# Kernel optimization log

Hardware: AMD Instinct MI355X
Metric: run time of the kernel (lower is better)

Reference implementation:

```python
import jax, jax.numpy as jnp
import numpy as np

B, C, W, H, D = 2, 256, 32, 32, 32
CH = C // 2  # 128
LN_EPS = 1e-5


def _spatial_pool(x, wm, bm):
    # x: [B,C,W,H,D]; wm: [C]; bm: scalar. 1x1x1 conv C->1 == channel dot.
    b, c = x.shape[0], x.shape[1]
    xf = x.reshape(b, c, -1)                       # [B,C,N]
    mask = jnp.einsum('bcn,c->bn', xf, wm) + bm    # [B,N]
    attn = jax.nn.softmax(mask, axis=1)            # softmax over spatial N
    return jnp.einsum('bcn,bn->bc', xf, attn)      # [B,C] weighted-sum pool


def _channel_add(ctx, w1, b1, g, be, w2, b2):
    # 1x1 conv C->C/2, LayerNorm over C/2, ReLU, 1x1 conv C/2->C
    h = ctx @ w1.T + b1                            # [B,CH]
    mu = jnp.mean(h, axis=-1, keepdims=True)
    var = jnp.mean((h - mu) ** 2, axis=-1, keepdims=True)
    h = (h - mu) * jax.lax.rsqrt(var + LN_EPS) * g + be
    h = jax.nn.relu(h)
    return h @ w2.T + b2                           # [B,C]


def setup_inputs() -> dict:
    key = jax.random.key(0)
    ks = jax.random.split(key, 20)
    s = 0.02
    d = {
        'preds_S': jax.random.normal(ks[0], (B, C, W, H, D), jnp.float32),
        'preds_T': jax.random.normal(ks[1], (B, C, W, H, D), jnp.float32),
        'wm_s': jax.random.normal(ks[2], (C,), jnp.float32) * s,
        'bm_s': jnp.zeros((), jnp.float32),
        'wm_t': jax.random.normal(ks[3], (C,), jnp.float32) * s,
        'bm_t': jnp.zeros((), jnp.float32),
        'w1_s': jax.random.normal(ks[4], (CH, C), jnp.float32) * s,
        'b1_s': jnp.zeros((CH,), jnp.float32),
        'g_s': jnp.ones((CH,), jnp.float32),
        'be_s': jnp.zeros((CH,), jnp.float32),
        'w2_s': jax.random.normal(ks[5], (C, CH), jnp.float32) * s,
        'b2_s': jnp.zeros((C,), jnp.float32),
        'w1_t': jax.random.normal(ks[6], (CH, C), jnp.float32) * s,
        'b1_t': jnp.zeros((CH,), jnp.float32),
        'g_t': jnp.ones((CH,), jnp.float32),
        'be_t': jnp.zeros((CH,), jnp.float32),
        'w2_t': jax.random.normal(ks[7], (C, CH), jnp.float32) * s,
        'b2_t': jnp.zeros((C,), jnp.float32),
    }
    return d


def reference(preds_S, preds_T, wm_s, bm_s, wm_t, bm_t,
              w1_s, b1_s, g_s, be_s, w2_s, b2_s,
              w1_t, b1_t, g_t, be_t, w2_t, b2_t):
    ctx_s = _spatial_pool(preds_S, wm_s, bm_s)     # [B,C]
    ctx_t = _spatial_pool(preds_T, wm_t, bm_t)
    add_s = _channel_add(ctx_s, w1_s, b1_s, g_s, be_s, w2_s, b2_s)  # [B,C]
    add_t = _channel_add(ctx_t, w1_t, b1_t, g_t, be_t, w2_t, b2_t)
    out_s = preds_S + add_s[:, :, None, None, None]
    out_t = preds_T + add_t[:, :, None, None, None]
    diff = out_s - out_t
    return jnp.sum(diff * diff) / preds_S.shape[0]
```

## Files before the change

kernel.cpp:

```cpp
#include <hip/hip_runtime.h>
#include <math.h>
#include <limits.h>

#define Bc   2
#define Cc   256
#define Nn   32768
#define CHc  128
#define NPC  8
#define CPB  (Cc / NPC)
#define NT   1024
#define NTILES (Nn / NT)
#define LN_EPS 1e-5f

__device__ __forceinline__ int enc_f(float f) {
  int i = __float_as_int(f);
  return i >= 0 ? i : (i ^ 0x7FFFFFFF);
}
__device__ __forceinline__ float dec_f(int k) {
  return __int_as_float(k >= 0 ? k : (k ^ 0x7FFFFFFF));
}

__global__ __launch_bounds__(256) void gc_k1_mask(
    const float* __restrict__ S, const float* __restrict__ T,
    const float* __restrict__ wms, const float* __restrict__ wmt,
    float* __restrict__ mp, int* __restrict__ Mkey,
    float* __restrict__ sumsq) {
  const int tile = blockIdx.x;
  const int b    = blockIdx.y;
  const int pc   = blockIdx.z;
  const int tid  = threadIdx.x;

  if (tile == 0 && b == 0 && pc == 0) {
    if (tid < 4) Mkey[tid] = INT_MIN;
    if (tid == 4) *sumsq = 0.f;
  }

  const int n0 = tile * NT + tid * 4;
  const int c0 = pc * CPB;

  const float* Sp = S + ((size_t)b * Cc + c0) * Nn + n0;
  const float* Tp = T + ((size_t)b * Cc + c0) * Nn + n0;

  float4 as = make_float4(0.f, 0.f, 0.f, 0.f);
  float4 at = make_float4(0.f, 0.f, 0.f, 0.f);

#pragma unroll 8
  for (int i = 0; i < CPB; ++i) {
    const float ws = wms[c0 + i];
    const float wt = wmt[c0 + i];
    const float4 s = *(const float4*)(Sp + (size_t)i * Nn);
    const float4 t = *(const float4*)(Tp + (size_t)i * Nn);
    as.x += ws * s.x; as.y += ws * s.y; as.z += ws * s.z; as.w += ws * s.w;
    at.x += wt * t.x; at.y += wt * t.y; at.z += wt * t.z; at.w += wt * t.w;
  }

  float* outS = mp + (((size_t)0 * NPC + pc) * Bc + b) * Nn + n0;
  float* outT = mp + (((size_t)1 * NPC + pc) * Bc + b) * Nn + n0;
  *(float4*)outS = as;
  *(float4*)outT = at;
}

__global__ __launch_bounds__(256) void gc_k2a_combine(
    const float* __restrict__ mp, const float* __restrict__ bms,
    const float* __restrict__ bmt, float* __restrict__ mask,
    int* __restrict__ Mkey) {
  const int tile = blockIdx.x;
  const int b    = blockIdx.y;
  const int tt   = blockIdx.z;
  const int tid  = threadIdx.x;
  const int n0   = tile * NT + tid * 4;

  const float bm = (tt ? bmt : bms)[0];
  float4 m = make_float4(bm, bm, bm, bm);
#pragma unroll
  for (int pc = 0; pc < NPC; ++pc) {
    const float4 p =
        *(const float4*)(mp + (((size_t)tt * NPC + pc) * Bc + b) * Nn + n0);
    m.x += p.x; m.y += p.y; m.z += p.z; m.w += p.w;
  }
  *(float4*)(mask + ((size_t)tt * Bc + b) * Nn + n0) = m;

  float lmax = fmaxf(fmaxf(m.x, m.y), fmaxf(m.z, m.w));
  __shared__ float red[256];
  red[tid] = lmax;
  __syncthreads();
  for (int s = 128; s > 0; s >>= 1) {
    if (tid < s) red[tid] = fmaxf(red[tid], red[tid + s]);
    __syncthreads();
  }
  if (tid == 0) atomicMax(&Mkey[tt * Bc + b], enc_f(red[0]));
}

__global__ __launch_bounds__(256) void gc_k3_pool(
    const float* __restrict__ S, const float* __restrict__ T,
    const float* __restrict__ mask, const int* __restrict__ Mkey,
    float* __restrict__ ctx, float* __restrict__ rowsum,
    float* __restrict__ sumsq) {
  const int c   = blockIdx.x;
  const int b   = blockIdx.y;
  const int tid = threadIdx.x;

  const float M1 = dec_f(Mkey[0 * Bc + b]);
  const float M2 = dec_f(Mkey[1 * Bc + b]);

  const float* Sp = S + ((size_t)b * Cc + c) * Nn;
  const float* Tp = T + ((size_t)b * Cc + c) * Nn;
  const float* m1 = mask + ((size_t)0 * Bc + b) * Nn;
  const float* m2 = mask + ((size_t)1 * Bc + b) * Nn;

  float cs = 0.f, ct = 0.f, te1 = 0.f, te2 = 0.f, rs = 0.f, sq = 0.f;
  for (int n = tid * 4; n < Nn; n += 1024) {
    const float4 s = *(const float4*)(Sp + n);
    const float4 t = *(const float4*)(Tp + n);
    const float4 a = *(const float4*)(m1 + n);
    const float4 g = *(const float4*)(m2 + n);
    const float e1x = __expf(a.x - M1), e1y = __expf(a.y - M1),
                e1z = __expf(a.z - M1), e1w = __expf(a.w - M1);
    const float e2x = __expf(g.x - M2), e2y = __expf(g.y - M2),
                e2z = __expf(g.z - M2), e2w = __expf(g.w - M2);
    cs += s.x * e1x + s.y * e1y + s.z * e1z + s.w * e1w;
    ct += t.x * e2x + t.y * e2y + t.z * e2z + t.w * e2w;
    te1 += e1x + e1y + e1z + e1w;
    te2 += e2x + e2y + e2z + e2w;
    const float dx = s.x - t.x, dy = s.y - t.y, dz = s.z - t.z, dw = s.w - t.w;
    rs += dx + dy + dz + dw;
    sq += dx * dx + dy * dy + dz * dz + dw * dw;
  }

  __shared__ float red[6][256];
  red[0][tid] = cs;  red[1][tid] = ct;  red[2][tid] = te1;
  red[3][tid] = te2; red[4][tid] = rs;  red[5][tid] = sq;
  __syncthreads();
  for (int s = 128; s > 0; s >>= 1) {
    if (tid < s) {
#pragma unroll
      for (int k = 0; k < 6; ++k) red[k][tid] += red[k][tid + s];
    }
    __syncthreads();
  }
  if (tid == 0) {
    ctx[((size_t)0 * Bc + b) * Cc + c] = red[0][0] / red[2][0];
    ctx[((size_t)1 * Bc + b) * Cc + c] = red[1][0] / red[3][0];
    rowsum[(size_t)b * Cc + c] = red[4][0];
    atomicAdd(sumsq, red[5][0]);
  }
}

__global__ __launch_bounds__(1024) void gc_k4a_mlp(
    const float* __restrict__ ctx,
    const float* __restrict__ w1s, const float* __restrict__ b1s,
    const float* __restrict__ gs,  const float* __restrict__ bes,
    const float* __restrict__ w2s, const float* __restrict__ b2s,
    const float* __restrict__ w1t, const float* __restrict__ b1t,
    const float* __restrict__ gt,  const float* __restrict__ bet,
    const float* __restrict__ w2t, const float* __restrict__ b2t,
    float* __restrict__ addv) {
  const int tt  = blockIdx.x >> 1;
  const int b   = blockIdx.x & 1;
  const int tid = threadIdx.x;

  const float* w1 = tt ? w1t : w1s;
  const float* b1 = tt ? b1t : b1s;
  const float* g  = tt ? gt  : gs;
  const float* be = tt ? bet : bes;
  const float* w2 = tt ? w2t : w2s;
  const float* b2 = tt ? b2t : b2s;

  __shared__ float cxs[Cc];
  __shared__ float part[1024];
  __shared__ float hbuf[CHc];
  __shared__ float hr[CHc];
  __shared__ float2 red2[128];
  __shared__ float mu_s, rstd_s;

  if (tid < Cc) cxs[tid] = ctx[((size_t)tt * Bc + b) * Cc + tid];
  __syncthreads();

  {
    const int j = tid >> 3, s = tid & 7;
    const float* wr = w1 + j * Cc + s * 32;
    const float4* cx4 = (const float4*)(cxs + s * 32);
    float acc = 0.f;
#pragma unroll
    for (int k = 0; k < 8; ++k) {
      const float4 w = *(const float4*)(wr + k * 4);
      const float4 x = cx4[k];
      acc += w.x * x.x + w.y * x.y + w.z * x.z + w.w * x.w;
    }
    part[tid] = acc;
  }
  __syncthreads();
  if (tid < CHc) {
    float h = b1[tid];
#pragma unroll
    for (int q = 0; q < 8; ++q) h += part[tid * 8 + q];
    hbuf[tid] = h;
  }
  __syncthreads();

  if (tid < CHc) {
    const float v = hbuf[tid];
    red2[tid] = make_float2(v, v * v);
  }
  __syncthreads();
  for (int s = 64; s > 0; s >>= 1) {
    if (tid < s) {
      red2[tid].x += red2[tid + s].x;
      red2[tid].y += red2[tid + s].y;
    }
    __syncthreads();
  }
  if (tid == 0) {
    const float mu = red2[0].x / (float)CHc;
    const float var = red2[0].y / (float)CHc - mu * mu;
    mu_s = mu;
    rstd_s = rsqrtf(var + LN_EPS);
  }
  __syncthreads();
  if (tid < CHc) {
    const float v = (hbuf[tid] - mu_s) * rstd_s * g[tid] + be[tid];
    hr[tid] = v > 0.f ? v : 0.f;
  }
  __syncthreads();

  {
    const int c = tid >> 2, q = tid & 3;
    const float* wr = w2 + c * CHc + q * 32;
    const float4* h4 = (const float4*)(hr + q * 32);
    float acc = 0.f;
#pragma unroll
    for (int k = 0; k < 8; ++k) {
      const float4 w = *(const float4*)(wr + k * 4);
      const float4 x = h4[k];
      acc += w.x * x.x + w.y * x.y + w.z * x.z + w.w * x.w;
    }
    part[tid] = acc;
  }
  __syncthreads();
  if (tid < Cc) {
    float acc = b2[tid];
#pragma unroll
    for (int q = 0; q < 4; ++q) acc += part[tid * 4 + q];
    addv[((size_t)tt * Bc + b) * Cc + tid] = acc;
  }
}

__global__ __launch_bounds__(256) void gc_k4b_final(
    const float* __restrict__ addv, const float* __restrict__ rowsum,
    const float* __restrict__ sumsq, float* __restrict__ out) {
  const int tid = threadIdx.x;
  __shared__ float red[256];
  float part = 0.f;
  for (int job = tid; job < Bc * Cc; job += 256) {
    const int c = job & (Cc - 1);
    const int b = job >> 8;
    const float delta = addv[((size_t)0 * Bc + b) * Cc + c] -
                        addv[((size_t)1 * Bc + b) * Cc + c];
    part += 2.f * delta * rowsum[(size_t)b * Cc + c] +
            (float)Nn * delta * delta;
  }
  red[tid] = part;
  __syncthreads();
  for (int s = 128; s > 0; s >>= 1) {
    if (tid < s) red[tid] += red[tid + s];
    __syncthreads();
  }
  if (tid == 0) out[0] = (red[0] + sumsq[0]) / (float)Bc;
}

extern "C" void kernel_launch(void* const* d_in, const int* in_sizes, int n_in,
                              void* d_out, int out_size, void* d_ws,
                              size_t ws_size, hipStream_t stream) {
  const float* S   = (const float*)d_in[0];
  const float* T   = (const float*)d_in[1];
  const float* wms = (const float*)d_in[2];
  const float* bms = (const float*)d_in[3];
  const float* wmt = (const float*)d_in[4];
  const float* bmt = (const float*)d_in[5];
  const float* w1s = (const float*)d_in[6];
  const float* b1s = (const float*)d_in[7];
  const float* gs  = (const float*)d_in[8];
  const float* bes = (const float*)d_in[9];
  const float* w2s = (const float*)d_in[10];
  const float* b2s = (const float*)d_in[11];
  const float* w1t = (const float*)d_in[12];
  const float* b1t = (const float*)d_in[13];
  const float* gt  = (const float*)d_in[14];
  const float* bet = (const float*)d_in[15];
  const float* w2t = (const float*)d_in[16];
  const float* b2t = (const float*)d_in[17];
  float* out = (float*)d_out;

  float* ws     = (float*)d_ws;
  float* mp     = ws;
  float* mask   = mp + (size_t)2 * NPC * Bc * Nn;
  float* ctx    = mask + (size_t)2 * Bc * Nn;
  float* rowsum = ctx + (size_t)2 * Bc * Cc;
  float* sumsq  = rowsum + (size_t)Bc * Cc;
  int*   Mkey   = (int*)(sumsq + 1);
  float* addv   = (float*)(Mkey + 4);

  gc_k1_mask<<<dim3(NTILES, Bc, NPC), 256, 0, stream>>>(S, T, wms, wmt, mp,
                                                        Mkey, sumsq);
  gc_k2a_combine<<<dim3(NTILES, Bc, 2), 256, 0, stream>>>(mp, bms, bmt, mask,
                                                          Mkey);
  gc_k3_pool<<<dim3(Cc, Bc), 256, 0, stream>>>(S, T, mask, Mkey, ctx, rowsum,
                                               sumsq);
  gc_k4a_mlp<<<4, 1024, 0, stream>>>(ctx, w1s, b1s, gs, bes, w2s, b2s, w1t,
                                     b1t, gt, bet, w2t, b2t, addv);
  gc_k4b_final<<<1, 256, 0, stream>>>(addv, rowsum, sumsq, out);
}
```

Before: 219.6 us.

## Split pool kernel over spatial halves and S/T mask passes across blocks

The mask kernel now handles S and T in separate blocks, doubling the grid, and uses two accumulators per thread. The pool kernel splits the spatial dimension in two and combines partial context sums, row sums and softmax denominators with atomics. Normalisation by the denominator moves into the MLP kernel. The goal is more blocks in flight to saturate HBM bandwidth, at the cost of extra atomics and zero-initialisation of the accumulators in the first kernel.

```diff
diff --git a/kernel.cpp b/kernel.cpp
--- a/kernel.cpp
+++ b/kernel.cpp
@@ -10,6 +10,7 @@
 #define CPB  (Cc / NPC)
 #define NT   1024
 #define NTILES (Nn / NT)
+#define NSPLIT 2
 #define LN_EPS 1e-5f
 
 __device__ __forceinline__ int enc_f(float f) {
@@ -24,40 +25,45 @@
     const float* __restrict__ S, const float* __restrict__ T,
     const float* __restrict__ wms, const float* __restrict__ wmt,
     float* __restrict__ mp, int* __restrict__ Mkey,
-    float* __restrict__ sumsq) {
+    float* __restrict__ sumsq, float* __restrict__ den,
+    float* __restrict__ ctxr, float* __restrict__ rowsum) {
   const int tile = blockIdx.x;
   const int b    = blockIdx.y;
-  const int pc   = blockIdx.z;
+  const int z    = blockIdx.z;
+  const int tt   = z >> 3;
+  const int pc   = z & (NPC - 1);
   const int tid  = threadIdx.x;
 
-  if (tile == 0 && b == 0 && pc == 0) {
-    if (tid < 4) Mkey[tid] = INT_MIN;
+  if (tile == 0 && b == 0 && z == 0) {
+    if (tid < 4) { Mkey[tid] = INT_MIN; den[tid] = 0.f; }
     if (tid == 4) *sumsq = 0.f;
+    for (int k = tid; k < 2 * Bc * Cc; k += 256) ctxr[k] = 0.f;
+    for (int k = tid; k < Bc * Cc; k += 256) rowsum[k] = 0.f;
   }
 
   const int n0 = tile * NT + tid * 4;
   const int c0 = pc * CPB;
 
-  const float* Sp = S + ((size_t)b * Cc + c0) * Nn + n0;
-  const float* Tp = T + ((size_t)b * Cc + c0) * Nn + n0;
-
-  float4 as = make_float4(0.f, 0.f, 0.f, 0.f);
-  float4 at = make_float4(0.f, 0.f, 0.f, 0.f);
-
-#pragma unroll 8
-  for (int i = 0; i < CPB; ++i) {
-    const float ws = wms[c0 + i];
-    const float wt = wmt[c0 + i];
-    const float4 s = *(const float4*)(Sp + (size_t)i * Nn);
-    const float4 t = *(const float4*)(Tp + (size_t)i * Nn);
-    as.x += ws * s.x; as.y += ws * s.y; as.z += ws * s.z; as.w += ws * s.w;
-    at.x += wt * t.x; at.y += wt * t.y; at.z += wt * t.z; at.w += wt * t.w;
-  }
-
-  float* outS = mp + (((size_t)0 * NPC + pc) * Bc + b) * Nn + n0;
-  float* outT = mp + (((size_t)1 * NPC + pc) * Bc + b) * Nn + n0;
-  *(float4*)outS = as;
-  *(float4*)outT = at;
+  const float* X  = tt ? T : S;
+  const float* wm = tt ? wmt : wms;
+  const float* Xp = X + ((size_t)b * Cc + c0) * Nn + n0;
+
+  float4 a0 = make_float4(0.f, 0.f, 0.f, 0.f);
+  float4 a1 = make_float4(0.f, 0.f, 0.f, 0.f);
+
+#pragma unroll 16
+  for (int i = 0; i < CPB; i += 2) {
+    const float w0 = wm[c0 + i];
+    const float w1 = wm[c0 + i + 1];
+    const float4 x0 = *(const float4*)(Xp + (size_t)i * Nn);
+    const float4 x1 = *(const float4*)(Xp + (size_t)(i + 1) * Nn);
+    a0.x += w0 * x0.x; a0.y += w0 * x0.y; a0.z += w0 * x0.z; a0.w += w0 * x0.w;
+    a1.x += w1 * x1.x; a1.y += w1 * x1.y; a1.z += w1 * x1.z; a1.w += w1 * x1.w;
+  }
+  a0.x += a1.x; a0.y += a1.y; a0.z += a1.z; a0.w += a1.w;
+
+  float* outp = mp + (((size_t)tt * NPC + pc) * Bc + b) * Nn + n0;
+  *(float4*)outp = a0;
 }
 
 __global__ __launch_bounds__(256) void gc_k2a_combine(
@@ -94,22 +100,25 @@
 __global__ __launch_bounds__(256) void gc_k3_pool(
     const float* __restrict__ S, const float* __restrict__ T,
     const float* __restrict__ mask, const int* __restrict__ Mkey,
-    float* __restrict__ ctx, float* __restrict__ rowsum,
-    float* __restrict__ sumsq) {
+    float* __restrict__ ctxr, float* __restrict__ rowsum,
+    float* __restrict__ sumsq, float* __restrict__ den) {
   const int c   = blockIdx.x;
   const int b   = blockIdx.y;
+  const int nh  = blockIdx.z;
   const int tid = threadIdx.x;
 
   const float M1 = dec_f(Mkey[0 * Bc + b]);
   const float M2 = dec_f(Mkey[1 * Bc + b]);
 
-  const float* Sp = S + ((size_t)b * Cc + c) * Nn;
-  const float* Tp = T + ((size_t)b * Cc + c) * Nn;
-  const float* m1 = mask + ((size_t)0 * Bc + b) * Nn;
-  const float* m2 = mask + ((size_t)1 * Bc + b) * Nn;
+  const int nbase = nh * (Nn / NSPLIT);
+  const float* Sp = S + ((size_t)b * Cc + c) * Nn + nbase;
+  const float* Tp = T + ((size_t)b * Cc + c) * Nn + nbase;
+  const float* m1 = mask + ((size_t)0 * Bc + b) * Nn + nbase;
+  const float* m2 = mask + ((size_t)1 * Bc + b) * Nn + nbase;
 
   float cs = 0.f, ct = 0.f, te1 = 0.f, te2 = 0.f, rs = 0.f, sq = 0.f;
-  for (int n = tid * 4; n < Nn; n += 1024) {
+#pragma unroll 4
+  for (int n = tid * 4; n < Nn / NSPLIT; n += 1024) {
     const float4 s = *(const float4*)(Sp + n);
     const float4 t = *(const float4*)(Tp + n);
     const float4 a = *(const float4*)(m1 + n);
@@ -139,15 +148,19 @@
     __syncthreads();
   }
   if (tid == 0) {
-    ctx[((size_t)0 * Bc + b) * Cc + c] = red[0][0] / red[2][0];
-    ctx[((size_t)1 * Bc + b) * Cc + c] = red[1][0] / red[3][0];
-    rowsum[(size_t)b * Cc + c] = red[4][0];
+    atomicAdd(&ctxr[((size_t)0 * Bc + b) * Cc + c], red[0][0]);
+    atomicAdd(&ctxr[((size_t)1 * Bc + b) * Cc + c], red[1][0]);
+    atomicAdd(&rowsum[(size_t)b * Cc + c], red[4][0]);
     atomicAdd(sumsq, red[5][0]);
+    if (c == 0) {
+      atomicAdd(&den[0 * Bc + b], red[2][0]);
+      atomicAdd(&den[1 * Bc + b], red[3][0]);
+    }
   }
 }
 
 __global__ __launch_bounds__(1024) void gc_k4a_mlp(
-    const float* __restrict__ ctx,
+    const float* __restrict__ ctxr, const float* __restrict__ den,
     const float* __restrict__ w1s, const float* __restrict__ b1s,
     const float* __restrict__ gs,  const float* __restrict__ bes,
     const float* __restrict__ w2s, const float* __restrict__ b2s,
@@ -173,7 +186,8 @@
   __shared__ float2 red2[128];
   __shared__ float mu_s, rstd_s;
 
-  if (tid < Cc) cxs[tid] = ctx[((size_t)tt * Bc + b) * Cc + tid];
+  if (tid < Cc)
+    cxs[tid] = ctxr[((size_t)tt * Bc + b) * Cc + tid] / den[tt * Bc + b];
   __syncthreads();
 
   {
@@ -294,19 +308,20 @@
   float* ws     = (float*)d_ws;
   float* mp     = ws;
   float* mask   = mp + (size_t)2 * NPC * Bc * Nn;
-  float* ctx    = mask + (size_t)2 * Bc * Nn;
-  float* rowsum = ctx + (size_t)2 * Bc * Cc;
+  float* ctxr   = mask + (size_t)2 * Bc * Nn;
+  float* rowsum = ctxr + (size_t)2 * Bc * Cc;
   float* sumsq  = rowsum + (size_t)Bc * Cc;
-  int*   Mkey   = (int*)(sumsq + 1);
+  float* den    = sumsq + 1;
+  int*   Mkey   = (int*)(den + 4);
   float* addv   = (float*)(Mkey + 4);
 
-  gc_k1_mask<<<dim3(NTILES, Bc, NPC), 256, 0, stream>>>(S, T, wms, wmt, mp,
-                                                        Mkey, sumsq);
+  gc_k1_mask<<<dim3(NTILES, Bc, 2 * NPC), 256, 0, stream>>>(
+      S, T, wms, wmt, mp, Mkey, sumsq, den, ctxr, rowsum);
   gc_k2a_combine<<<dim3(NTILES, Bc, 2), 256, 0, stream>>>(mp, bms, bmt, mask,
                                                           Mkey);
-  gc_k3_pool<<<dim3(Cc, Bc), 256, 0, stream>>>(S, T, mask, Mkey, ctx, rowsum,
-                                               sumsq);
-  gc_k4a_mlp<<<4, 1024, 0, stream>>>(ctx, w1s, b1s, gs, bes, w2s, b2s, w1t,
-                                     b1t, gt, bet, w2t, b2t, addv);
+  gc_k3_pool<<<dim3(Cc, Bc, NSPLIT), 256, 0, stream>>>(S, T, mask, Mkey, ctxr,
+                                                       rowsum, sumsq, den);
+  gc_k4a_mlp<<<4, 1024, 0, stream>>>(ctxr, den, w1s, b1s, gs, bes, w2s, b2s,
+                                     w1t, b1t, gt, bet, w2t, b2t, addv);
   gc_k4b_final<<<1, 256, 0, stream>>>(addv, rowsum, sumsq, out);
 }
```

After: 224.0 us. About the same (+2.0%).

## Fuse mask, softmax pool and diff reductions into one streaming pass

Applied to the files above, without the earlier changes.

Replaces the mask, combine and pool kernels with one fused kernel. Each block computes the channel-dot mask for a spatial tile through a shared-memory reduction across channel groups, exponentiates it, and accumulates the weighted pool numerators, denominators, row sums and squared differences, which are merged with global atomics. S and T are therefore read once instead of twice, and the intermediate mask buffers disappear. In exchange the softmax no longer subtracts the running max, so exp can overflow if mask values are large. Float atomics also make the accumulation order nondeterministic, and a memset is added to zero the accumulators.

```diff
diff --git a/kernel.cpp b/kernel.cpp
--- a/kernel.cpp
+++ b/kernel.cpp
@@ -1,153 +1,160 @@
 #include <hip/hip_runtime.h>
 #include <math.h>
-#include <limits.h>
 
 #define Bc   2
 #define Cc   256
 #define Nn   32768
 #define CHc  128
-#define NPC  8
-#define CPB  (Cc / NPC)
-#define NT   1024
-#define NTILES (Nn / NT)
 #define LN_EPS 1e-5f
 
-__device__ __forceinline__ int enc_f(float f) {
-  int i = __float_as_int(f);
-  return i >= 0 ? i : (i ^ 0x7FFFFFFF);
-}
-__device__ __forceinline__ float dec_f(int k) {
-  return __int_as_float(k >= 0 ? k : (k ^ 0x7FFFFFFF));
-}
-
-__global__ __launch_bounds__(256) void gc_k1_mask(
+#define TN    64
+#define TPB   512
+#define NQ    16
+#define CG    32
+#define CPG   8
+#define TPBLK 2
+#define GRIDX (Nn / (TN * TPBLK))
+
+__global__ __launch_bounds__(TPB) void gc_fused(
     const float* __restrict__ S, const float* __restrict__ T,
-    const float* __restrict__ wms, const float* __restrict__ wmt,
-    float* __restrict__ mp, int* __restrict__ Mkey,
+    const float* __restrict__ wms, const float* __restrict__ bms,
+    const float* __restrict__ wmt, const float* __restrict__ bmt,
+    float* __restrict__ ctxnum,
+    float* __restrict__ rowsum,
+    float* __restrict__ den,
     float* __restrict__ sumsq) {
-  const int tile = blockIdx.x;
-  const int b    = blockIdx.y;
-  const int pc   = blockIdx.z;
-  const int tid  = threadIdx.x;
-
-  if (tile == 0 && b == 0 && pc == 0) {
-    if (tid < 4) Mkey[tid] = INT_MIN;
-    if (tid == 4) *sumsq = 0.f;
-  }
-
-  const int n0 = tile * NT + tid * 4;
-  const int c0 = pc * CPB;
-
-  const float* Sp = S + ((size_t)b * Cc + c0) * Nn + n0;
-  const float* Tp = T + ((size_t)b * Cc + c0) * Nn + n0;
-
-  float4 as = make_float4(0.f, 0.f, 0.f, 0.f);
-  float4 at = make_float4(0.f, 0.f, 0.f, 0.f);
-
-#pragma unroll 8
-  for (int i = 0; i < CPB; ++i) {
-    const float ws = wms[c0 + i];
-    const float wt = wmt[c0 + i];
-    const float4 s = *(const float4*)(Sp + (size_t)i * Nn);
-    const float4 t = *(const float4*)(Tp + (size_t)i * Nn);
-    as.x += ws * s.x; as.y += ws * s.y; as.z += ws * s.z; as.w += ws * s.w;
-    at.x += wt * t.x; at.y += wt * t.y; at.z += wt * t.z; at.w += wt * t.w;
-  }
-
-  float* outS = mp + (((size_t)0 * NPC + pc) * Bc + b) * Nn + n0;
-  float* outT = mp + (((size_t)1 * NPC + pc) * Bc + b) * Nn + n0;
-  *(float4*)outS = as;
-  *(float4*)outT = at;
-}
-
-__global__ __launch_bounds__(256) void gc_k2a_combine(
-    const float* __restrict__ mp, const float* __restrict__ bms,
-    const float* __restrict__ bmt, float* __restrict__ mask,
-    int* __restrict__ Mkey) {
-  const int tile = blockIdx.x;
-  const int b    = blockIdx.y;
-  const int tt   = blockIdx.z;
-  const int tid  = threadIdx.x;
-  const int n0   = tile * NT + tid * 4;
-
-  const float bm = (tt ? bmt : bms)[0];
-  float4 m = make_float4(bm, bm, bm, bm);
-#pragma unroll
-  for (int pc = 0; pc < NPC; ++pc) {
-    const float4 p =
-        *(const float4*)(mp + (((size_t)tt * NPC + pc) * Bc + b) * Nn + n0);
-    m.x += p.x; m.y += p.y; m.z += p.z; m.w += p.w;
-  }
-  *(float4*)(mask + ((size_t)tt * Bc + b) * Nn + n0) = m;
-
-  float lmax = fmaxf(fmaxf(m.x, m.y), fmaxf(m.z, m.w));
-  __shared__ float red[256];
-  red[tid] = lmax;
-  __syncthreads();
-  for (int s = 128; s > 0; s >>= 1) {
-    if (tid < s) red[tid] = fmaxf(red[tid], red[tid + s]);
-    __syncthreads();
-  }
-  if (tid == 0) atomicMax(&Mkey[tt * Bc + b], enc_f(red[0]));
-}
-
-__global__ __launch_bounds__(256) void gc_k3_pool(
-    const float* __restrict__ S, const float* __restrict__ T,
-    const float* __restrict__ mask, const int* __restrict__ Mkey,
-    float* __restrict__ ctx, float* __restrict__ rowsum,
-    float* __restrict__ sumsq) {
-  const int c   = blockIdx.x;
   const int b   = blockIdx.y;
   const int tid = threadIdx.x;
-
-  const float M1 = dec_f(Mkey[0 * Bc + b]);
-  const float M2 = dec_f(Mkey[1 * Bc + b]);
-
-  const float* Sp = S + ((size_t)b * Cc + c) * Nn;
-  const float* Tp = T + ((size_t)b * Cc + c) * Nn;
-  const float* m1 = mask + ((size_t)0 * Bc + b) * Nn;
-  const float* m2 = mask + ((size_t)1 * Bc + b) * Nn;
-
-  float cs = 0.f, ct = 0.f, te1 = 0.f, te2 = 0.f, rs = 0.f, sq = 0.f;
-  for (int n = tid * 4; n < Nn; n += 1024) {
-    const float4 s = *(const float4*)(Sp + n);
-    const float4 t = *(const float4*)(Tp + n);
-    const float4 a = *(const float4*)(m1 + n);
-    const float4 g = *(const float4*)(m2 + n);
-    const float e1x = __expf(a.x - M1), e1y = __expf(a.y - M1),
-                e1z = __expf(a.z - M1), e1w = __expf(a.w - M1);
-    const float e2x = __expf(g.x - M2), e2y = __expf(g.y - M2),
-                e2z = __expf(g.z - M2), e2w = __expf(g.w - M2);
-    cs += s.x * e1x + s.y * e1y + s.z * e1z + s.w * e1w;
-    ct += t.x * e2x + t.y * e2y + t.z * e2z + t.w * e2w;
-    te1 += e1x + e1y + e1z + e1w;
-    te2 += e2x + e2y + e2z + e2w;
-    const float dx = s.x - t.x, dy = s.y - t.y, dz = s.z - t.z, dw = s.w - t.w;
-    rs += dx + dy + dz + dw;
-    sq += dx * dx + dy * dy + dz * dz + dw * dw;
-  }
-
-  __shared__ float red[6][256];
-  red[0][tid] = cs;  red[1][tid] = ct;  red[2][tid] = te1;
-  red[3][tid] = te2; red[4][tid] = rs;  red[5][tid] = sq;
-  __syncthreads();
-  for (int s = 128; s > 0; s >>= 1) {
-    if (tid < s) {
-#pragma unroll
-      for (int k = 0; k < 6; ++k) red[k][tid] += red[k][tid + s];
-    }
-    __syncthreads();
-  }
+  const int nq  = tid & (NQ - 1);
+  const int cg  = tid >> 4;
+  const int c0  = cg * CPG;
+
+  __shared__ float4 mred[2][CG][NQ];
+  __shared__ float  cred[Cc * 17];
+
+  float wS[CPG], wT[CPG];
+#pragma unroll
+  for (int i = 0; i < CPG; ++i) { wS[i] = wms[c0 + i]; wT[i] = wmt[c0 + i]; }
+  const float bS = bms[0];
+  const float bT = bmt[0];
+
+  float cs[CPG], ct[CPG], rs[CPG];
+#pragma unroll
+  for (int i = 0; i < CPG; ++i) { cs[i] = 0.f; ct[i] = 0.f; rs[i] = 0.f; }
+  float sq = 0.f, pden_s = 0.f, pden_t = 0.f;
+
+  for (int it = 0; it < TPBLK; ++it) {
+    const int n0 = (blockIdx.x * TPBLK + it) * TN + nq * 4;
+    const float* Sp = S + ((size_t)b * Cc + c0) * Nn + n0;
+    const float* Tp = T + ((size_t)b * Cc + c0) * Nn + n0;
+
+    float4 s4[CPG], t4[CPG];
+#pragma unroll
+    for (int i = 0; i < CPG; ++i) s4[i] = *(const float4*)(Sp + (size_t)i * Nn);
+#pragma unroll
+    for (int i = 0; i < CPG; ++i) t4[i] = *(const float4*)(Tp + (size_t)i * Nn);
+
+    float4 ms = make_float4(0.f, 0.f, 0.f, 0.f);
+    float4 mt = make_float4(0.f, 0.f, 0.f, 0.f);
+#pragma unroll
+    for (int i = 0; i < CPG; ++i) {
+      ms.x += wS[i] * s4[i].x; ms.y += wS[i] * s4[i].y;
+      ms.z += wS[i] * s4[i].z; ms.w += wS[i] * s4[i].w;
+      mt.x += wT[i] * t4[i].x; mt.y += wT[i] * t4[i].y;
+      mt.z += wT[i] * t4[i].z; mt.w += wT[i] * t4[i].w;
+      const float dx = s4[i].x - t4[i].x, dy = s4[i].y - t4[i].y;
+      const float dz = s4[i].z - t4[i].z, dw = s4[i].w - t4[i].w;
+      rs[i] += dx + dy + dz + dw;
+      sq += dx * dx + dy * dy + dz * dz + dw * dw;
+    }
+
+    __syncthreads();
+    mred[0][cg][nq] = ms;
+    mred[1][cg][nq] = mt;
+    __syncthreads();
+#pragma unroll
+    for (int st = CG / 2; st > 0; st >>= 1) {
+      if (cg < st) {
+        const float4 a0 = mred[0][cg][nq], a1 = mred[0][cg + st][nq];
+        mred[0][cg][nq] =
+            make_float4(a0.x + a1.x, a0.y + a1.y, a0.z + a1.z, a0.w + a1.w);
+        const float4 b0 = mred[1][cg][nq], b1 = mred[1][cg + st][nq];
+        mred[1][cg][nq] =
+            make_float4(b0.x + b1.x, b0.y + b1.y, b0.z + b1.z, b0.w + b1.w);
+      }
+      __syncthreads();
+    }
+    const float4 Ms = mred[0][0][nq];
+    const float4 Mt = mred[1][0][nq];
+    float4 es, et;
+    es.x = __expf(Ms.x + bS); es.y = __expf(Ms.y + bS);
+    es.z = __expf(Ms.z + bS); es.w = __expf(Ms.w + bS);
+    et.x = __expf(Mt.x + bT); et.y = __expf(Mt.y + bT);
+    et.z = __expf(Mt.z + bT); et.w = __expf(Mt.w + bT);
+
+    if (cg == 0) {
+      pden_s += es.x + es.y + es.z + es.w;
+      pden_t += et.x + et.y + et.z + et.w;
+    }
+#pragma unroll
+    for (int i = 0; i < CPG; ++i) {
+      cs[i] += s4[i].x * es.x + s4[i].y * es.y + s4[i].z * es.z + s4[i].w * es.w;
+      ct[i] += t4[i].x * et.x + t4[i].y * et.y + t4[i].z * et.z + t4[i].w * et.w;
+    }
+  }
+
+  __syncthreads();
+#pragma unroll
+  for (int i = 0; i < CPG; ++i) cred[(c0 + i) * 17 + nq] = cs[i];
+  __syncthreads();
+  if (tid < Cc) {
+    float v = 0.f;
+#pragma unroll
+    for (int k = 0; k < NQ; ++k) v += cred[tid * 17 + k];
+    atomicAdd(&ctxnum[((size_t)0 * Bc + b) * Cc + tid], v);
+  }
+  __syncthreads();
+#pragma unroll
+  for (int i = 0; i < CPG; ++i) cred[(c0 + i) * 17 + nq] = ct[i];
+  __syncthreads();
+  if (tid < Cc) {
+    float v = 0.f;
+#pragma unroll
+    for (int k = 0; k < NQ; ++k) v += cred[tid * 17 + k];
+    atomicAdd(&ctxnum[((size_t)1 * Bc + b) * Cc + tid], v);
+  }
+  __syncthreads();
+#pragma unroll
+  for (int i = 0; i < CPG; ++i) cred[(c0 + i) * 17 + nq] = rs[i];
+  __syncthreads();
+  if (tid < Cc) {
+    float v = 0.f;
+#pragma unroll
+    for (int k = 0; k < NQ; ++k) v += cred[tid * 17 + k];
+    atomicAdd(&rowsum[(size_t)b * Cc + tid], v);
+  }
+  __syncthreads();
+  cred[tid] = sq;
+  __syncthreads();
+  for (int st = TPB / 2; st > 0; st >>= 1) {
+    if (tid < st) cred[tid] += cred[tid + st];
+    __syncthreads();
+  }
+  if (tid == 0) atomicAdd(sumsq, cred[0]);
+  __syncthreads();
+  if (tid < NQ) { cred[tid] = pden_s; cred[NQ + tid] = pden_t; }
+  __syncthreads();
   if (tid == 0) {
-    ctx[((size_t)0 * Bc + b) * Cc + c] = red[0][0] / red[2][0];
-    ctx[((size_t)1 * Bc + b) * Cc + c] = red[1][0] / red[3][0];
-    rowsum[(size_t)b * Cc + c] = red[4][0];
-    atomicAdd(sumsq, red[5][0]);
+    float a = 0.f, c = 0.f;
+#pragma unroll
+    for (int k = 0; k < NQ; ++k) { a += cred[k]; c += cred[NQ + k]; }
+    atomicAdd(&den[0 * Bc + b], a);
+    atomicAdd(&den[1 * Bc + b], c);
   }
 }
 
 __global__ __launch_bounds__(1024) void gc_k4a_mlp(
-    const float* __restrict__ ctx,
+    const float* __restrict__ ctxr, const float* __restrict__ den,
     const float* __restrict__ w1s, const float* __restrict__ b1s,
     const float* __restrict__ gs,  const float* __restrict__ bes,
     const float* __restrict__ w2s, const float* __restrict__ b2s,
@@ -173,7 +180,8 @@
   __shared__ float2 red2[128];
   __shared__ float mu_s, rstd_s;
 
-  if (tid < Cc) cxs[tid] = ctx[((size_t)tt * Bc + b) * Cc + tid];
+  if (tid < Cc)
+    cxs[tid] = ctxr[((size_t)tt * Bc + b) * Cc + tid] / den[tt * Bc + b];
   __syncthreads();
 
   {
@@ -292,21 +300,18 @@
   float* out = (float*)d_out;
 
   float* ws     = (float*)d_ws;
-  float* mp     = ws;
-  float* mask   = mp + (size_t)2 * NPC * Bc * Nn;
-  float* ctx    = mask + (size_t)2 * Bc * Nn;
-  float* rowsum = ctx + (size_t)2 * Bc * Cc;
-  float* sumsq  = rowsum + (size_t)Bc * Cc;
-  int*   Mkey   = (int*)(sumsq + 1);
-  float* addv   = (float*)(Mkey + 4);
-
-  gc_k1_mask<<<dim3(NTILES, Bc, NPC), 256, 0, stream>>>(S, T, wms, wmt, mp,
-                                                        Mkey, sumsq);
-  gc_k2a_combine<<<dim3(NTILES, Bc, 2), 256, 0, stream>>>(mp, bms, bmt, mask,
-                                                          Mkey);
-  gc_k3_pool<<<dim3(Cc, Bc), 256, 0, stream>>>(S, T, mask, Mkey, ctx, rowsum,
-                                               sumsq);
-  gc_k4a_mlp<<<4, 1024, 0, stream>>>(ctx, w1s, b1s, gs, bes, w2s, b2s, w1t,
-                                     b1t, gt, bet, w2t, b2t, addv);
+  float* ctxnum = ws;
+  float* rowsum = ctxnum + 2 * Bc * Cc;
+  float* den    = rowsum + Bc * Cc;
+  float* sumsq  = den + 4;
+  float* addv   = sumsq + 1;
+
+  hipMemsetAsync(d_ws, 0, (2 * Bc * Cc + Bc * Cc + 4 + 1) * sizeof(float),
+                 stream);
+
+  gc_fused<<<dim3(GRIDX, Bc), TPB, 0, stream>>>(S, T, wms, bms, wmt, bmt,
+                                                ctxnum, rowsum, den, sumsq);
+  gc_k4a_mlp<<<4, 1024, 0, stream>>>(ctxnum, den, w1s, b1s, gs, bes, w2s, b2s,
+                                     w1t, b1t, gt, bet, w2t, b2t, addv);
   gc_k4b_final<<<1, 256, 0, stream>>>(addv, rowsum, sumsq, out);
 }
```

Measured after the change: 207.9 us. 5.3% less time.
